# Optimization experiments

Measured on AMD Instinct MI355X. Metric: run time of the kernel, lower is better.

Reference implementation:

```python
import jax, jax.numpy as jnp
import numpy as np

N, E = 100000, 640000
IN, H, C, L = 128, 128, 64, 5
BN_EPS = 1e-5


def setup_inputs() -> dict:
    key = jax.random.key(0)
    ks = jax.random.split(key, 12)
    x = jax.random.normal(ks[0], (N, IN), jnp.float32)
    edge_index = jax.random.randint(ks[1], (2, E), 0, N, dtype=jnp.int64)
    # GCNConv weights: layer0 in->hidden, layers 1..4 hidden->hidden
    W_in = jax.random.normal(ks[2], (IN, H), jnp.float32) / np.sqrt(IN).astype(np.float32)
    b_in = jnp.zeros((H,), jnp.float32)
    Ws = jax.random.normal(ks[3], (L - 1, H, H), jnp.float32) / np.sqrt(H).astype(np.float32)
    bs = jnp.zeros((L - 1, H), jnp.float32)
    # BatchNorm1d (eval mode) params per layer
    gammas = jnp.ones((L, H), jnp.float32)
    betas = jnp.zeros((L, H), jnp.float32)
    run_mean = 0.1 * jax.random.normal(ks[4], (L, H), jnp.float32)
    run_var = jax.random.uniform(ks[5], (L, H), jnp.float32) + 0.5
    # final node-level classifier
    W_out = jax.random.normal(ks[6], (H, C), jnp.float32) / np.sqrt(H).astype(np.float32)
    b_out = jnp.zeros((C,), jnp.float32)
    return {"x": x, "edge_index": edge_index, "W_in": W_in, "b_in": b_in,
            "Ws": Ws, "bs": bs, "gammas": gammas, "betas": betas,
            "run_mean": run_mean, "run_var": run_var, "W_out": W_out, "b_out": b_out}


def reference(x, edge_index, W_in, b_in, Ws, bs, gammas, betas, run_mean, run_var, W_out, b_out):
    src, dst = edge_index[0], edge_index[1]
    n = x.shape[0]
    # GCN symmetric norm with self-loops: deg counts incoming edges + 1
    deg = jax.ops.segment_sum(jnp.ones(src.shape, x.dtype), dst, num_segments=n) + 1.0
    dis = jax.lax.rsqrt(deg)                      # deg^{-1/2}, [N]
    coef = dis[src] * dis[dst]                    # per-edge norm, [E]
    self_coef = (dis * dis)[:, None]              # self-loop norm deg^{-1}, [N,1]

    h = x
    for l in range(L):
        W = W_in if l == 0 else Ws[l - 1]
        b = b_in if l == 0 else bs[l - 1]
        t = h @ W                                 # [N,H]
        agg = jax.ops.segment_sum(t[src] * coef[:, None], dst, num_segments=n)
        agg = agg + t * self_coef + b             # neighbor agg + self loop + bias
        # BatchNorm1d in eval mode (running stats)
        y = (agg - run_mean[l]) * jax.lax.rsqrt(run_var[l] + BN_EPS) * gammas[l] + betas[l]
        h = jax.nn.relu(y)                        # dropout is identity in eval
    return h @ W_out + b_out                      # [N, num_classes]
```

## Files before the change

kernel.cpp:

```cpp
#include <hip/hip_runtime.h>
#include <cstdint>

#define BN_EPS 1e-5f

typedef __bf16 bf16x8 __attribute__((ext_vector_type(8)));
typedef __bf16 bf16x4 __attribute__((ext_vector_type(4)));
typedef __bf16 bf16x2 __attribute__((ext_vector_type(2)));
typedef float f32x4 __attribute__((ext_vector_type(4)));


__global__ __launch_bounds__(256) void k_count(const int* __restrict__ dstv,
                                               int* __restrict__ counts,
                                               int* __restrict__ rank, int E) {
  int e = blockIdx.x * 256 + threadIdx.x;
  if (e < E) rank[e] = atomicAdd(counts + dstv[e], 1);
}

__global__ __launch_bounds__(256) void k_dis(const int* __restrict__ counts,
                                             float* __restrict__ dis, int N) {
  int i = blockIdx.x * 256 + threadIdx.x;
  if (i < N) dis[i] = rsqrtf((float)counts[i] + 1.0f);
}

__global__ __launch_bounds__(256) void k_scan1(const int* __restrict__ counts,
                                               int* __restrict__ rowstart,
                                               int* __restrict__ bsum, int N) {
  __shared__ int wsum[4];
  const int tid = threadIdx.x, lane = tid & 63, wv = tid >> 6;
  const int base = blockIdx.x * 1024 + tid * 4;
  int c[4];
#pragma unroll
  for (int j = 0; j < 4; ++j) {
    int idx = base + j;
    c[j] = (idx < N) ? counts[idx] : 0;
  }
  int s = c[0] + c[1] + c[2] + c[3];
  int x = s;
  for (int d = 1; d < 64; d <<= 1) {
    int y = __shfl_up(x, d);
    if (lane >= d) x += y;
  }
  if (lane == 63) wsum[wv] = x;
  __syncthreads();
  int woff = 0;
  for (int w = 0; w < wv; ++w) woff += wsum[w];
  int r = woff + x - s;
#pragma unroll
  for (int j = 0; j < 4; ++j) {
    int idx = base + j;
    if (idx < N) rowstart[idx] = r;
    r += c[j];
  }
  if (tid == 255) bsum[blockIdx.x] = woff + x;
}

__global__ __launch_bounds__(256) void k_scan2(const int* __restrict__ bsum,
                                               int* __restrict__ boff, int nb) {
  __shared__ int sm[256];
  const int tid = threadIdx.x;
  int v = (tid < nb) ? bsum[tid] : 0;
  sm[tid] = v;
  __syncthreads();
  for (int d = 1; d < 256; d <<= 1) {
    int y = (tid >= d) ? sm[tid - d] : 0;
    __syncthreads();
    sm[tid] += y;
    __syncthreads();
  }
  if (tid < nb) boff[tid] = sm[tid] - v;
}

__global__ __launch_bounds__(256) void k_fix(int* __restrict__ rowstart,
                                             const int* __restrict__ boff, int N) {
  int i = blockIdx.x * 256 + threadIdx.x;
  if (i < N) rowstart[i] += boff[i >> 10];
}

__global__ __launch_bounds__(256) void k_scatter(const int* __restrict__ src,
                                                 const int* __restrict__ dstv,
                                                 const int* __restrict__ rowstart,
                                                 const int* __restrict__ rank,
                                                 int* __restrict__ esrc, int E) {
  int e = blockIdx.x * 256 + threadIdx.x;
  if (e < E) esrc[rowstart[dstv[e]] + rank[e]] = src[e];
}

__global__ __launch_bounds__(256) void k_bnparam(const float* __restrict__ gamma,
                                                 const float* __restrict__ beta,
                                                 const float* __restrict__ mean,
                                                 const float* __restrict__ var,
                                                 float* __restrict__ scale,
                                                 float* __restrict__ shift, int n) {
  int i = blockIdx.x * 256 + threadIdx.x;
  if (i < n) {
    float s = gamma[i] * rsqrtf(var[i] + BN_EPS);
    scale[i] = s;
    shift[i] = beta[i] - mean[i] * s;
  }
}

__global__ __launch_bounds__(64) void k_zrow(__bf16* __restrict__ t, int N) {
  bf16x2 z;
  z[0] = (__bf16)0.f;
  z[1] = (__bf16)0.f;
  *reinterpret_cast<bf16x2*>(t + (size_t)N * 128 + threadIdx.x * 2) = z;
}

__global__ __launch_bounds__(256) void k_wprep(const float* __restrict__ W_in,
                                               const float* __restrict__ Ws,
                                               const float* __restrict__ W_out,
                                               __bf16* __restrict__ wfrag) {
  const int idx = blockIdx.x * 256 + threadIdx.x;
  if (idx >= 11264) return;
  int l, r, CT;
  if (idx < 10240) { l = idx >> 11; r = idx & 2047; CT = 8; }
  else             { l = 5; r = idx - 10240; CT = 4; }
  const int lane = r & 63;
  const int rr = r >> 6;
  const int ct = rr % CT;
  const int kc_i = rr / CT;
  const int lr = lane & 15, kg = lane >> 4;
  const int col = ct * 16 + lr;
  const int k0 = kc_i * 32 + kg * 8;
  const float* Wsrc;
  int ncols;
  if (l == 0)      { Wsrc = W_in; ncols = 128; }
  else if (l <= 4) { Wsrc = Ws + (size_t)(l - 1) * 16384; ncols = 128; }
  else             { Wsrc = W_out; ncols = 64; }
  bf16x8 hi, lo;
#pragma unroll
  for (int j = 0; j < 8; ++j) {
    float v = Wsrc[(size_t)(k0 + j) * ncols + col];
    __bf16 h = (__bf16)v;
    hi[j] = h;
    lo[j] = (__bf16)(v - (float)h);
  }
  const size_t lbase = (l < 5) ? (size_t)l * 65536 : (size_t)327680;
  char* outp = (char*)wfrag + lbase;
  *(bf16x8*)(outp + ((size_t)(kc_i * 2 + 0) * CT + ct) * 1024 + lane * 16) = hi;
  *(bf16x8*)(outp + ((size_t)(kc_i * 2 + 1) * CT + ct) * 1024 + lane * 16) = lo;
}

template <int BNC, bool A_FP32, bool FINAL>
__global__ __launch_bounds__(256, 4) void k_mgemm(
    const void* __restrict__ in_v, const __bf16* __restrict__ wfrag,
    const float* __restrict__ dis, const float* __restrict__ out_bias,
    float* __restrict__ outf, __bf16* __restrict__ outh, int N) {
  constexpr int CT = BNC / 16;
  __shared__ __align__(16) char Abase[32768];

  const int tid = threadIdx.x;
  const int lane = tid & 63;
  const int wv = tid >> 6;
  const int lr = lane & 15;
  const int kg = lane >> 4;
  const int rowBase = blockIdx.x * 128;

  if constexpr (A_FP32) {
    const float* in = (const float*)in_v;
    const int kq = tid & 31;
#pragma unroll
    for (int i = 0; i < 16; ++i) {
      const int row = (tid >> 5) + i * 8;
      const int grow = rowBase + row;
      float4 v = make_float4(0.f, 0.f, 0.f, 0.f);
      if (grow < N) v = *(const float4*)(in + (size_t)grow * 128 + kq * 4);
      bf16x4 h;
      h[0] = (__bf16)v.x; h[1] = (__bf16)v.y; h[2] = (__bf16)v.z; h[3] = (__bf16)v.w;
      int byte = row * 256 + kq * 8;
      byte ^= (row & 7) << 4;
      *(bf16x4*)(Abase + byte) = h;
    }
  } else {
    const __bf16* in = (const __bf16*)in_v;
    const int kq = tid & 15;
#pragma unroll
    for (int i = 0; i < 8; ++i) {
      const int row = (tid >> 4) + i * 16;
      const int grow = rowBase + row;
      uint4 v = make_uint4(0, 0, 0, 0);
      if (grow < N) v = *(const uint4*)(in + (size_t)grow * 128 + kq * 8);
      int byte = row * 256 + kq * 16;
      byte ^= (row & 7) << 4;
      *(uint4*)(Abase + byte) = v;
    }
  }
  __syncthreads();

  f32x4 acc[2][CT] = {};

#pragma unroll
  for (int kc_i = 0; kc_i < 4; ++kc_i) {
    bf16x8 afr[2];
#pragma unroll
    for (int rt = 0; rt < 2; ++rt) {
      const int row = wv * 32 + rt * 16 + lr;
      int byte = row * 256 + kc_i * 64 + kg * 16;
      byte ^= (row & 7) << 4;
      afr[rt] = *(const bf16x8*)(Abase + byte);
    }
    const char* wk = (const char*)wfrag + (size_t)kc_i * (2 * CT * 1024) +
                     (size_t)lane * 16;
#pragma unroll
    for (int ct = 0; ct < CT; ++ct) {
      bf16x8 bhi = *(const bf16x8*)(wk + ct * 1024);
      bf16x8 blo = *(const bf16x8*)(wk + (CT + ct) * 1024);
#pragma unroll
      for (int rt = 0; rt < 2; ++rt) {
        acc[rt][ct] = __builtin_amdgcn_mfma_f32_16x16x32_bf16(afr[rt], bhi,
                                                              acc[rt][ct], 0, 0, 0);
        acc[rt][ct] = __builtin_amdgcn_mfma_f32_16x16x32_bf16(afr[rt], blo,
                                                              acc[rt][ct], 0, 0, 0);
      }
    }
  }

  float ob[CT];
  if constexpr (FINAL) {
#pragma unroll
    for (int ct = 0; ct < CT; ++ct) ob[ct] = out_bias[ct * 16 + lr];
  }
#pragma unroll
  for (int rt = 0; rt < 2; ++rt) {
#pragma unroll
    for (int j = 0; j < 4; ++j) {
      const int row = rowBase + wv * 32 + rt * 16 + kg * 4 + j;
      if (row < N) {
        if constexpr (FINAL) {
#pragma unroll
          for (int ct = 0; ct < CT; ++ct)
            outf[(size_t)row * BNC + ct * 16 + lr] = acc[rt][ct][j] + ob[ct];
        } else {
          const float dr = dis[row];
#pragma unroll
          for (int ct = 0; ct < CT; ++ct)
            outh[(size_t)row * BNC + ct * 16 + lr] = (__bf16)(acc[rt][ct][j] * dr);
        }
      }
    }
  }
}

__global__ __launch_bounds__(256) void k_agg(const int* __restrict__ rowstart,
                                             const int* __restrict__ counts,
                                             const int* __restrict__ esrc,
                                             const __bf16* __restrict__ t,
                                             const float* __restrict__ dis,
                                             const float* __restrict__ bias,
                                             const float* __restrict__ scale,
                                             const float* __restrict__ shift,
                                             __bf16* __restrict__ h, int N) {
  const int lane = threadIdx.x & 63;
  const int wv = threadIdx.x >> 6;
  const int node = blockIdx.x * 4 + wv;
  if (node >= N) return;
  const int beg = rowstart[node];
  const int cnt = counts[node];
  const float dn = dis[node];

  bf16x2 sv = *reinterpret_cast<const bf16x2*>(t + (size_t)node * 128 + lane * 2);
  int rec = (lane < cnt) ? esrc[beg + lane] : N;

  float ax = (float)sv[0];
  float ay = (float)sv[1];

  const int m = cnt < 64 ? cnt : 64;
  const int rounds = (m + 7) >> 3;
  for (int r = 0; r < rounds; ++r) {
    const int base = r * 8;
#pragma unroll
    for (int u = 0; u < 8; ++u) {
      const int s = __builtin_amdgcn_readlane(rec, base + u);
      const bf16x2 v =
          *reinterpret_cast<const bf16x2*>(t + (size_t)s * 128 + lane * 2);
      ax += (float)v[0];
      ay += (float)v[1];
    }
  }
  for (int i = 64; i < cnt; ++i) {
    const int s0 = esrc[beg + i];
    const bf16x2 v0 =
        *reinterpret_cast<const bf16x2*>(t + (size_t)s0 * 128 + lane * 2);
    ax += (float)v0[0];
    ay += (float)v0[1];
  }

  ax = fmaf(ax, dn, bias[lane * 2 + 0]);
  ay = fmaf(ay, dn, bias[lane * 2 + 1]);
  ax = fmaxf(fmaf(ax, scale[lane * 2 + 0], shift[lane * 2 + 0]), 0.f);
  ay = fmaxf(fmaf(ay, scale[lane * 2 + 1], shift[lane * 2 + 1]), 0.f);
  bf16x2 o;
  o[0] = (__bf16)ax;
  o[1] = (__bf16)ay;
  *reinterpret_cast<bf16x2*>(h + (size_t)node * 128 + lane * 2) = o;
}

extern "C" void kernel_launch(void* const* d_in, const int* in_sizes, int n_in,
                              void* d_out, int out_size, void* d_ws, size_t ws_size,
                              hipStream_t stream) {
  const float* x      = (const float*)d_in[0];
  const int*   ei     = (const int*)d_in[1];
  const float* W_in   = (const float*)d_in[2];
  const float* b_in   = (const float*)d_in[3];
  const float* Ws     = (const float*)d_in[4];
  const float* bs     = (const float*)d_in[5];
  const float* gammas = (const float*)d_in[6];
  const float* betas  = (const float*)d_in[7];
  const float* mean   = (const float*)d_in[8];
  const float* var    = (const float*)d_in[9];
  const float* W_out  = (const float*)d_in[10];
  const float* b_out  = (const float*)d_in[11];
  float* out = (float*)d_out;

  const int N = in_sizes[0] / 128;
  const int E = in_sizes[1] / 2;
  const int* src = ei;
  const int* dst = ei + E;

  char* ws = (char*)d_ws;
  size_t off = 0;
  auto alloc = [&](size_t bytes) {
    void* p = ws + off;
    off = (off + bytes + 255) & ~255ULL;
    return p;
  };
  int*    counts   = (int*)alloc((size_t)N * 4);
  int*    rowstart = (int*)alloc((size_t)N * 4);
  int*    bsum     = (int*)alloc(256 * 4);
  int*    boff     = (int*)alloc(256 * 4);
  float*  dis      = (float*)alloc((size_t)N * 4);
  float*  scale    = (float*)alloc(5 * 128 * 4);
  float*  shift    = (float*)alloc(5 * 128 * 4);
  __bf16* wfrag    = (__bf16*)alloc(360448);
  int*    rank     = (int*)alloc((size_t)E * 4);
  int*    esrc     = (int*)alloc((size_t)E * 4);
  __bf16* t        = (__bf16*)alloc(((size_t)N + 1) * 128 * 2);
  __bf16* h        = (__bf16*)alloc((size_t)N * 128 * 2);
  (void)ws_size;

  const int nb = (N + 1023) / 1024;

  hipMemsetAsync(counts, 0, (size_t)N * 4, stream);
  k_count<<<(E + 255) / 256, 256, 0, stream>>>(dst, counts, rank, E);
  k_dis<<<(N + 255) / 256, 256, 0, stream>>>(counts, dis, N);
  k_scan1<<<nb, 256, 0, stream>>>(counts, rowstart, bsum, N);
  k_scan2<<<1, 256, 0, stream>>>(bsum, boff, nb);
  k_fix<<<(N + 255) / 256, 256, 0, stream>>>(rowstart, boff, N);
  k_scatter<<<(E + 255) / 256, 256, 0, stream>>>(src, dst, rowstart, rank, esrc, E);
  k_bnparam<<<(5 * 128 + 255) / 256, 256, 0, stream>>>(gammas, betas, mean, var,
                                                       scale, shift, 5 * 128);
  k_wprep<<<44, 256, 0, stream>>>(W_in, Ws, W_out, wfrag);
  k_zrow<<<1, 64, 0, stream>>>(t, N);

  const int gblocks = (N + 127) / 128;
  const int ablocks = (N + 3) / 4;

  k_mgemm<128, true, false><<<gblocks, 256, 0, stream>>>(
      x, wfrag, dis, nullptr, nullptr, t, N);

  const float* biases[5] = {b_in, bs, bs + 128, bs + 256, bs + 384};
  for (int l = 0; l < 4; ++l) {
    k_agg<<<ablocks, 256, 0, stream>>>(rowstart, counts, esrc, t, dis, biases[l],
                                       scale + l * 128, shift + l * 128, h, N);
    k_mgemm<128, false, false><<<gblocks, 256, 0, stream>>>(
        h, wfrag + (size_t)(l + 1) * 32768, dis, nullptr, nullptr, t, N);
  }
  k_agg<<<ablocks, 256, 0, stream>>>(rowstart, counts, esrc, t, dis, biases[4],
                                     scale + 4 * 128, shift + 4 * 128, h, N);
  k_mgemm<64, false, true><<<gblocks, 256, 0, stream>>>(
      h, wfrag + 163840, nullptr, b_out, out, nullptr, N);
}
```

Before: 354.2 us.

## Fuse neighbor aggregation into following GEMM via LDS staging

Replaces the separate aggregation kernel and GEMM with a single per-layer kernel. Each wave aggregates 32 nodes, writes the normalized, BN'd and ReLU'd rows straight into the swizzled LDS A tile, then runs the MFMA GEMM on it. This removes the global round trip of the intermediate h buffer and half of the kernel launches. Ping-pong t buffers replace the single t/h pair. The cost is lower parallelism in the gather phase: one wave now walks 32 nodes serially, prefetching the next node's edge list, instead of one wave per node.

```diff
diff --git a/kernel.cpp b/kernel.cpp
--- a/kernel.cpp
+++ b/kernel.cpp
@@ -141,12 +141,10 @@
   *(bf16x8*)(outp + ((size_t)(kc_i * 2 + 1) * CT + ct) * 1024 + lane * 16) = lo;
 }
 
-template <int BNC, bool A_FP32, bool FINAL>
-__global__ __launch_bounds__(256, 4) void k_mgemm(
-    const void* __restrict__ in_v, const __bf16* __restrict__ wfrag,
-    const float* __restrict__ dis, const float* __restrict__ out_bias,
-    float* __restrict__ outf, __bf16* __restrict__ outh, int N) {
-  constexpr int CT = BNC / 16;
+__global__ __launch_bounds__(256, 4) void k_mgemm0(
+    const float* __restrict__ in, const __bf16* __restrict__ wfrag,
+    const float* __restrict__ dis, __bf16* __restrict__ outh, int N) {
+  constexpr int CT = 8;
   __shared__ __align__(16) char Abase[32768];
 
   const int tid = threadIdx.x;
@@ -156,8 +154,7 @@
   const int kg = lane >> 4;
   const int rowBase = blockIdx.x * 128;
 
-  if constexpr (A_FP32) {
-    const float* in = (const float*)in_v;
+  {
     const int kq = tid & 31;
 #pragma unroll
     for (int i = 0; i < 16; ++i) {
@@ -171,24 +168,10 @@
       byte ^= (row & 7) << 4;
       *(bf16x4*)(Abase + byte) = h;
     }
-  } else {
-    const __bf16* in = (const __bf16*)in_v;
-    const int kq = tid & 15;
-#pragma unroll
-    for (int i = 0; i < 8; ++i) {
-      const int row = (tid >> 4) + i * 16;
-      const int grow = rowBase + row;
-      uint4 v = make_uint4(0, 0, 0, 0);
-      if (grow < N) v = *(const uint4*)(in + (size_t)grow * 128 + kq * 8);
-      int byte = row * 256 + kq * 16;
-      byte ^= (row & 7) << 4;
-      *(uint4*)(Abase + byte) = v;
-    }
   }
   __syncthreads();
 
   f32x4 acc[2][CT] = {};
-
 #pragma unroll
   for (int kc_i = 0; kc_i < 4; ++kc_i) {
     bf16x8 afr[2];
@@ -215,6 +198,138 @@
     }
   }
 
+#pragma unroll
+  for (int rt = 0; rt < 2; ++rt) {
+#pragma unroll
+    for (int j = 0; j < 4; ++j) {
+      const int row = rowBase + wv * 32 + rt * 16 + kg * 4 + j;
+      if (row < N) {
+        const float dr = dis[row];
+#pragma unroll
+        for (int ct = 0; ct < CT; ++ct)
+          outh[(size_t)row * 128 + ct * 16 + lr] = (__bf16)(acc[rt][ct][j] * dr);
+      }
+    }
+  }
+}
+
+template <int CT, bool FINAL>
+__global__ __launch_bounds__(256, 4) void k_layer(
+    const __bf16* __restrict__ tin, const __bf16* __restrict__ wfrag,
+    const int* __restrict__ rowstart, const int* __restrict__ counts,
+    const int* __restrict__ esrc, const float* __restrict__ dis,
+    const float* __restrict__ bias, const float* __restrict__ scale,
+    const float* __restrict__ shift, const float* __restrict__ out_bias,
+    float* __restrict__ outf, __bf16* __restrict__ outh, int N) {
+  __shared__ __align__(16) char Abase[32768];
+
+  const int tid = threadIdx.x;
+  const int lane = tid & 63;
+  const int wv = tid >> 6;
+  const int lr = lane & 15;
+  const int kg = lane >> 4;
+  const int rowBase = blockIdx.x * 128;
+
+  {
+    const int nb0 = rowBase + wv * 32;
+    int mb = 0, mc = 0, mdbits = 0;
+    if (lane < 32) {
+      const int nd = nb0 + lane;
+      if (nd < N) {
+        mb = rowstart[nd];
+        mc = counts[nd];
+        mdbits = __float_as_int(dis[nd]);
+      }
+    }
+    const int f0 = lane * 2;
+    const float bx = bias[f0], by = bias[f0 + 1];
+    const float scx = scale[f0], scy = scale[f0 + 1];
+    const float shx = shift[f0], shy = shift[f0 + 1];
+
+    int ci = __builtin_amdgcn_readlane(mc, 0);
+    int rec = (lane < ci) ? esrc[__builtin_amdgcn_readlane(mb, 0) + lane] : N;
+
+    for (int i = 0; i < 32; ++i) {
+      const int node = nb0 + i;
+      const float dn = __int_as_float(__builtin_amdgcn_readlane(mdbits, i));
+      const int srow = (node < N) ? node : N;
+      const bf16x2 sv =
+          *reinterpret_cast<const bf16x2*>(tin + (size_t)srow * 128 + f0);
+      int rec_n = N, cn = 0;
+      if (i < 31) {
+        const int bn_ = __builtin_amdgcn_readlane(mb, i + 1);
+        cn = __builtin_amdgcn_readlane(mc, i + 1);
+        if (lane < cn) rec_n = esrc[bn_ + lane];
+      }
+      float ax = (float)sv[0];
+      float ay = (float)sv[1];
+      const int m = ci < 64 ? ci : 64;
+      const int rounds = (m + 7) >> 3;
+      for (int r = 0; r < rounds; ++r) {
+        const int rb = r * 8;
+#pragma unroll
+        for (int u = 0; u < 8; ++u) {
+          const int s = __builtin_amdgcn_readlane(rec, rb + u);
+          const bf16x2 v =
+              *reinterpret_cast<const bf16x2*>(tin + (size_t)s * 128 + f0);
+          ax += (float)v[0];
+          ay += (float)v[1];
+        }
+      }
+      if (__builtin_expect(ci > 64, 0)) {
+        const int bi = __builtin_amdgcn_readlane(mb, i);
+        for (int e = 64; e < ci; ++e) {
+          const int s0 = esrc[bi + e];
+          const bf16x2 v0 =
+              *reinterpret_cast<const bf16x2*>(tin + (size_t)s0 * 128 + f0);
+          ax += (float)v0[0];
+          ay += (float)v0[1];
+        }
+      }
+      ax = fmaf(ax, dn, bx);
+      ay = fmaf(ay, dn, by);
+      ax = fmaxf(fmaf(ax, scx, shx), 0.f);
+      ay = fmaxf(fmaf(ay, scy, shy), 0.f);
+      bf16x2 o;
+      o[0] = (__bf16)ax;
+      o[1] = (__bf16)ay;
+      const int row = wv * 32 + i;
+      int byte = row * 256 + lane * 4;
+      byte ^= (row & 7) << 4;
+      *(bf16x2*)(Abase + byte) = o;
+      rec = rec_n;
+      ci = cn;
+    }
+  }
+  __syncthreads();
+
+  f32x4 acc[2][CT] = {};
+#pragma unroll
+  for (int kc_i = 0; kc_i < 4; ++kc_i) {
+    bf16x8 afr[2];
+#pragma unroll
+    for (int rt = 0; rt < 2; ++rt) {
+      const int row = wv * 32 + rt * 16 + lr;
+      int byte = row * 256 + kc_i * 64 + kg * 16;
+      byte ^= (row & 7) << 4;
+      afr[rt] = *(const bf16x8*)(Abase + byte);
+    }
+    const char* wk = (const char*)wfrag + (size_t)kc_i * (2 * CT * 1024) +
+                     (size_t)lane * 16;
+#pragma unroll
+    for (int ct = 0; ct < CT; ++ct) {
+      bf16x8 bhi = *(const bf16x8*)(wk + ct * 1024);
+      bf16x8 blo = *(const bf16x8*)(wk + (CT + ct) * 1024);
+#pragma unroll
+      for (int rt = 0; rt < 2; ++rt) {
+        acc[rt][ct] = __builtin_amdgcn_mfma_f32_16x16x32_bf16(afr[rt], bhi,
+                                                              acc[rt][ct], 0, 0, 0);
+        acc[rt][ct] = __builtin_amdgcn_mfma_f32_16x16x32_bf16(afr[rt], blo,
+                                                              acc[rt][ct], 0, 0, 0);
+      }
+    }
+  }
+
   float ob[CT];
   if constexpr (FINAL) {
 #pragma unroll
@@ -229,70 +344,16 @@
         if constexpr (FINAL) {
 #pragma unroll
           for (int ct = 0; ct < CT; ++ct)
-            outf[(size_t)row * BNC + ct * 16 + lr] = acc[rt][ct][j] + ob[ct];
+            outf[(size_t)row * (CT * 16) + ct * 16 + lr] = acc[rt][ct][j] + ob[ct];
         } else {
           const float dr = dis[row];
 #pragma unroll
           for (int ct = 0; ct < CT; ++ct)
-            outh[(size_t)row * BNC + ct * 16 + lr] = (__bf16)(acc[rt][ct][j] * dr);
+            outh[(size_t)row * 128 + ct * 16 + lr] = (__bf16)(acc[rt][ct][j] * dr);
         }
       }
     }
   }
-}
-
-__global__ __launch_bounds__(256) void k_agg(const int* __restrict__ rowstart,
-                                             const int* __restrict__ counts,
-                                             const int* __restrict__ esrc,
-                                             const __bf16* __restrict__ t,
-                                             const float* __restrict__ dis,
-                                             const float* __restrict__ bias,
-                                             const float* __restrict__ scale,
-                                             const float* __restrict__ shift,
-                                             __bf16* __restrict__ h, int N) {
-  const int lane = threadIdx.x & 63;
-  const int wv = threadIdx.x >> 6;
-  const int node = blockIdx.x * 4 + wv;
-  if (node >= N) return;
-  const int beg = rowstart[node];
-  const int cnt = counts[node];
-  const float dn = dis[node];
-
-  bf16x2 sv = *reinterpret_cast<const bf16x2*>(t + (size_t)node * 128 + lane * 2);
-  int rec = (lane < cnt) ? esrc[beg + lane] : N;
-
-  float ax = (float)sv[0];
-  float ay = (float)sv[1];
-
-  const int m = cnt < 64 ? cnt : 64;
-  const int rounds = (m + 7) >> 3;
-  for (int r = 0; r < rounds; ++r) {
-    const int base = r * 8;
-#pragma unroll
-    for (int u = 0; u < 8; ++u) {
-      const int s = __builtin_amdgcn_readlane(rec, base + u);
-      const bf16x2 v =
-          *reinterpret_cast<const bf16x2*>(t + (size_t)s * 128 + lane * 2);
-      ax += (float)v[0];
-      ay += (float)v[1];
-    }
-  }
-  for (int i = 64; i < cnt; ++i) {
-    const int s0 = esrc[beg + i];
-    const bf16x2 v0 =
-        *reinterpret_cast<const bf16x2*>(t + (size_t)s0 * 128 + lane * 2);
-    ax += (float)v0[0];
-    ay += (float)v0[1];
-  }
-
-  ax = fmaf(ax, dn, bias[lane * 2 + 0]);
-  ay = fmaf(ay, dn, bias[lane * 2 + 1]);
-  ax = fmaxf(fmaf(ax, scale[lane * 2 + 0], shift[lane * 2 + 0]), 0.f);
-  ay = fmaxf(fmaf(ay, scale[lane * 2 + 1], shift[lane * 2 + 1]), 0.f);
-  bf16x2 o;
-  o[0] = (__bf16)ax;
-  o[1] = (__bf16)ay;
-  *reinterpret_cast<bf16x2*>(h + (size_t)node * 128 + lane * 2) = o;
 }
 
 extern "C" void kernel_launch(void* const* d_in, const int* in_sizes, int n_in,
@@ -334,8 +395,8 @@
   __bf16* wfrag    = (__bf16*)alloc(360448);
   int*    rank     = (int*)alloc((size_t)E * 4);
   int*    esrc     = (int*)alloc((size_t)E * 4);
-  __bf16* t        = (__bf16*)alloc(((size_t)N + 1) * 128 * 2);
-  __bf16* h        = (__bf16*)alloc((size_t)N * 128 * 2);
+  __bf16* tA       = (__bf16*)alloc(((size_t)N + 1) * 128 * 2);
+  __bf16* tB       = (__bf16*)alloc(((size_t)N + 1) * 128 * 2);
   (void)ws_size;
 
   const int nb = (N + 1023) / 1024;
@@ -350,23 +411,26 @@
   k_bnparam<<<(5 * 128 + 255) / 256, 256, 0, stream>>>(gammas, betas, mean, var,
                                                        scale, shift, 5 * 128);
   k_wprep<<<44, 256, 0, stream>>>(W_in, Ws, W_out, wfrag);
-  k_zrow<<<1, 64, 0, stream>>>(t, N);
+  k_zrow<<<1, 64, 0, stream>>>(tA, N);
+  k_zrow<<<1, 64, 0, stream>>>(tB, N);
 
   const int gblocks = (N + 127) / 128;
-  const int ablocks = (N + 3) / 4;
-
-  k_mgemm<128, true, false><<<gblocks, 256, 0, stream>>>(
-      x, wfrag, dis, nullptr, nullptr, t, N);
+
+  k_mgemm0<<<gblocks, 256, 0, stream>>>(x, wfrag, dis, tA, N);
 
   const float* biases[5] = {b_in, bs, bs + 128, bs + 256, bs + 384};
-  for (int l = 0; l < 4; ++l) {
-    k_agg<<<ablocks, 256, 0, stream>>>(rowstart, counts, esrc, t, dis, biases[l],
-                                       scale + l * 128, shift + l * 128, h, N);
-    k_mgemm<128, false, false><<<gblocks, 256, 0, stream>>>(
-        h, wfrag + (size_t)(l + 1) * 32768, dis, nullptr, nullptr, t, N);
-  }
-  k_agg<<<ablocks, 256, 0, stream>>>(rowstart, counts, esrc, t, dis, biases[4],
-                                     scale + 4 * 128, shift + 4 * 128, h, N);
-  k_mgemm<64, false, true><<<gblocks, 256, 0, stream>>>(
-      h, wfrag + 163840, nullptr, b_out, out, nullptr, N);
-}
+  __bf16* tin = tA;
+  __bf16* tout = tB;
+  for (int l = 1; l <= 4; ++l) {
+    k_layer<8, false><<<gblocks, 256, 0, stream>>>(
+        tin, wfrag + (size_t)l * 32768, rowstart, counts, esrc, dis,
+        biases[l - 1], scale + (l - 1) * 128, shift + (l - 1) * 128, nullptr,
+        nullptr, tout, N);
+    __bf16* tmp = tin;
+    tin = tout;
+    tout = tmp;
+  }
+  k_layer<4, true><<<gblocks, 256, 0, stream>>>(
+      tin, wfrag + 163840, rowstart, counts, esrc, dis, biases[4],
+      scale + 4 * 128, shift + 4 * 128, b_out, out, nullptr, N);
+}
```

Result: faster. 334.5 us (-5.6%).
